# Kernel tuning notes

Hardware: AMD Instinct MI355X
Metric: run time of the kernel (lower is better)

Reference implementation:

```python
import jax, jax.numpy as jnp
import numpy as np

C = 32        # channels
B = 4         # batch
H = W = 256   # spatial
K = 3         # adaptive kernel size
BN_EPS = 1e-5


def conv2d(x, w, b, pad):
    # x: [B,Cin,H,W], w: [Cout,Cin,kh,kw]
    y = jax.lax.conv_general_dilated(
        x, w, window_strides=(1, 1), padding=[(pad, pad), (pad, pad)],
        dimension_numbers=('NCHW', 'OIHW', 'NCHW'))
    return y + b[None, :, None, None]


def bn(x, g, beta, mu, var):
    scale = (g / jnp.sqrt(var + BN_EPS))[None, :, None, None]
    return (x - mu[None, :, None, None]) * scale + beta[None, :, None, None]


def res_block(x, w, b, g, beta, mu, var):
    # w: [2,C,C,3,3]; conv-BN-ReLU-conv-BN, residual add, ReLU
    h = bn(conv2d(x, w[0], b[0], 1), g[0], beta[0], mu[0], var[0])
    h = jax.nn.relu(h)
    h = bn(conv2d(h, w[1], b[1], 1), g[1], beta[1], mu[1], var[1])
    return jax.nn.relu(x + h)


def kernel_pred(frames, core, rate):
    # frames: [B,N,H,W] (color=1 squeezed), core: [B,N,K*K,H,W]
    b, n, h, w = frames.shape
    p = (K // 2) * rate
    fp = jnp.pad(frames, ((0, 0), (0, 0), (p, p), (p, p)))
    # stack K*K shifted copies along new axis 2 (same order as torch loop)
    stack = jnp.stack([fp[:, :, i * rate:i * rate + h, j * rate:j * rate + w]
                       for i in range(K) for j in range(K)], axis=2)
    return jnp.sum(core * stack, axis=2)  # [B,N,H,W]; white_level=1.0


def setup_inputs() -> dict:
    key = jax.random.key(0)
    ks = jax.random.split(key, 16)
    inp = {}
    inp['input'] = jax.random.normal(ks[0], (B, C, H, W), dtype=jnp.float32)
    # 4 residual blocks x 2 convs each
    inp['wconv'] = 0.05 * jax.random.normal(ks[1], (4, 2, C, C, 3, 3), dtype=jnp.float32)
    inp['bconv'] = jnp.zeros((4, 2, C), dtype=jnp.float32)
    inp['bn_gamma'] = jnp.ones((4, 2, C), dtype=jnp.float32) + 0.01 * jax.random.normal(ks[2], (4, 2, C), dtype=jnp.float32)
    inp['bn_beta'] = 0.01 * jax.random.normal(ks[3], (4, 2, C), dtype=jnp.float32)
    inp['bn_mean'] = 0.1 * jax.random.normal(ks[4], (4, 2, C), dtype=jnp.float32)
    inp['bn_var'] = 0.5 + jax.random.uniform(ks[5], (4, 2, C), dtype=jnp.float32)
    inp['tau'] = 0.5 * jnp.ones((1, C, 1, 1), dtype=jnp.float32)
    inp['w_outc'] = 0.05 * jax.random.normal(ks[6], (C * 9, C, 1, 1), dtype=jnp.float32)
    inp['b_outc'] = jnp.zeros((C * 9,), dtype=jnp.float32)
    inp['w_final'] = 0.05 * jax.random.normal(ks[7], (C, C * 4, 3, 3), dtype=jnp.float32)
    inp['b_final'] = jnp.zeros((C,), dtype=jnp.float32)
    return inp


def reference(input, wconv, bconv, bn_gamma, bn_beta, bn_mean, bn_var, tau,
              w_outc, b_outc, w_final, b_final):
    m = input
    for i in range(4):  # fixed small structural loop over residual blocks
        m = res_block(m, wconv[i], bconv[i], bn_gamma[i], bn_beta[i],
                      bn_mean[i], bn_var[i])
    m5 = jax.nn.relu(m - tau)
    core = conv2d(m5, w_outc, b_outc, 0)                    # [B, C*9, H, W]
    core = core.reshape(B, C, K * K, H, W)                  # [B, N, 9, H, W]
    preds = [kernel_pred(input, core, r) for r in (1, 2, 3, 4)]
    pred_cat = jnp.concatenate(preds, axis=1)               # [B, 4C, H, W]
    return conv2d(pred_cat, w_final, b_final, 1)            # [B, C, H, W]
```

## Files before the change

### kernel.cpp

```cpp
#include <hip/hip_runtime.h>

typedef __bf16 bf16;
typedef __attribute__((ext_vector_type(8))) __bf16 bf16x8;
typedef __attribute__((ext_vector_type(4))) float f32x4;

#define HH 256
#define WW 256
#define BB 4
#define NPIX 65536
#define AS 264
#define APX 69696
#define PS 258
#define PPX 66564

#define GLOAD16(SRC, DST) __builtin_amdgcn_global_load_lds( \
    (const __attribute__((address_space(1))) void*)(SRC),   \
    (__attribute__((address_space(3))) void*)(DST), 16, 0, 0)

__device__ inline bf16x8 bzero8() {
    bf16x8 v;
    #pragma unroll
    for (int i = 0; i < 8; ++i) v[i] = (bf16)0.0f;
    return v;
}

__device__ inline int chof(int s) {
    return 4 * (s >> 3) + 16 * ((s >> 2) & 1) + (s & 3);
}

__global__ __launch_bounds__(256) void prep_in(const float* __restrict__ in,
                                               bf16* __restrict__ outP) {
    int p = blockIdx.x * 256 + threadIdx.x;
    int b = p >> 16, rem = p & 65535;
    int y = rem >> 8, x = rem & 255;
    float ch[32];
    #pragma unroll
    for (int c = 0; c < 32; ++c)
        ch[c] = in[(size_t)(b * 32 + c) * NPIX + rem];
    bf16* o = outP + ((size_t)b * APX + (size_t)(y + 4) * AS + x + 4) * 32;
    #pragma unroll
    for (int g = 0; g < 4; ++g) {
        bf16x8 w;
        #pragma unroll
        for (int j = 0; j < 4; ++j) {
            w[j]     = (bf16)ch[4 * g + j];
            w[4 + j] = (bf16)ch[16 + 4 * g + j];
        }
        *reinterpret_cast<bf16x8*>(o + g * 8) = w;
    }
}

__global__ __launch_bounds__(256) void zero_halo(bf16* __restrict__ in0b,
                                                 bf16* __restrict__ actA,
                                                 bf16* __restrict__ actB,
                                                 bf16* __restrict__ pred) {
    int i = blockIdx.x * 256 + threadIdx.x;
    const int NA = 3 * 4 * 4160;
    if (i < NA) {
        int buf = i / (4 * 4160), r = i % (4 * 4160);
        int b = r / 4160, k = r % 4160;
        int y, x;
        if (k < 2112) { int rr = k / 264; y = rr < 4 ? rr : 256 + rr; x = k % 264; }
        else { int j = k - 2112; y = 4 + j / 8; int c8 = j % 8; x = c8 < 4 ? c8 : 256 + c8; }
        bf16* p = (buf == 0 ? in0b : buf == 1 ? actA : actB) +
                  ((size_t)b * APX + (size_t)y * AS + x) * 32;
        #pragma unroll
        for (int cg = 0; cg < 4; ++cg)
            *reinterpret_cast<bf16x8*>(p + cg * 8) = bzero8();
    } else if (i < NA + 4 * 1028) {
        int r = i - NA;
        int b = r / 1028, k = r % 1028;
        int y, x;
        if (k < 516) { int rr = k / 258; y = rr ? 257 : 0; x = k % 258; }
        else { int j = k - 516; y = 1 + j / 2; x = (j & 1) ? 257 : 0; }
        bf16* p = pred + ((size_t)b * PPX + (size_t)y * PS + x) * 128;
        #pragma unroll
        for (int cg = 0; cg < 16; ++cg)
            *reinterpret_cast<bf16x8*>(p + cg * 8) = bzero8();
    }
}

__global__ void fold_w(const float* __restrict__ wconv, const float* __restrict__ bconv,
                       const float* __restrict__ g, const float* __restrict__ beta,
                       const float* __restrict__ mu, const float* __restrict__ var,
                       const float* __restrict__ w_outc, const float* __restrict__ b_outc,
                       const float* __restrict__ w_final, const float* __restrict__ tau,
                       bf16* __restrict__ Wres, float* __restrict__ Bres,
                       bf16* __restrict__ Wcore, bf16* __restrict__ Wfin,
                       float* __restrict__ bCore, float* __restrict__ tauP) {
    int idx = blockIdx.x * 256 + threadIdx.x;
    if (idx < 73728) {
        int l = idx / 9216, r = idx % 9216;
        int tap = r >> 10, co = (r >> 5) & 31, ci = chof(r & 31);
        float s = g[l * 32 + co] * rsqrtf(var[l * 32 + co] + 1e-5f);
        Wres[idx] = (bf16)(wconv[l * 9216 + (co * 32 + ci) * 9 + tap] * s);
    } else if (idx < 73984) {
        int i = idx - 73728;
        float s = g[i] * rsqrtf(var[i] + 1e-5f);
        Bres[i] = (bconv[i] - mu[i]) * s + beta[i];
    } else if (idx < 83200) {
        int r = idx - 73984;
        int tap = r >> 10, nn = (r >> 5) & 31, ci = chof(r & 31);
        Wcore[r] = (bf16)w_outc[(nn * 9 + tap) * 32 + ci];
    } else if (idx < 120064) {
        int r = idx - 83200;
        int chunk = r / 9216, r2 = r % 9216;
        int tap = r2 >> 10, co = (r2 >> 5) & 31, n = chof(r2 & 31);
        Wfin[r] = (bf16)w_final[(size_t)(co * 128 + chunk * 32 + n) * 9 + tap];
    } else if (idx < 120352) {
        int r = idx - 120064;
        int tap = r >> 5, n = r & 31;
        bCore[r] = b_outc[n * 9 + tap];
    } else if (idx < 120384) {
        int s = idx - 120352;
        tauP[s] = tau[chof(s)];
    }
}

__global__ __launch_bounds__(512) void resblock_v4(
    const bf16* __restrict__ in, const bf16* __restrict__ W1,
    const bf16* __restrict__ W2, const float* __restrict__ B1,
    const float* __restrict__ B2, bf16* __restrict__ out) {
    extern __shared__ char smem[];
    bf16* xs = (bf16*)smem;
    bf16* hs = (bf16*)(smem + 52224);
    const int x0 = blockIdx.x * 64, y0 = blockIdx.y * 8, b = blockIdx.z;
    const int tid = threadIdx.x;
    const int lane = tid & 63, wv = tid >> 6;
    const int col = lane & 15, g = lane >> 4;
    const bf16* inb = in + (size_t)b * APX * 32;

    for (int gi = wv; gi < 51; gi += 8) {
        int i = gi * 64 + lane;
        int px = i >> 2, s = i & 3;
        int yy = px / 68, xx = px % 68;
        int gsl = s ^ ((px >> 1) & 3);
        const bf16* src = inb + ((size_t)(y0 + yy + 2) * AS + x0 + xx + 2) * 32 + gsl * 8;
        GLOAD16(src, smem + gi * 1024);
    }

    bf16x8 Wf[9][2];
    #pragma unroll
    for (int tap = 0; tap < 9; ++tap) {
        Wf[tap][0] = *reinterpret_cast<const bf16x8*>(W1 + tap * 1024 + col * 32 + g * 8);
        Wf[tap][1] = *reinterpret_cast<const bf16x8*>(W1 + tap * 1024 + (16 + col) * 32 + g * 8);
    }
    f32x4 bb0 = *reinterpret_cast<const f32x4*>(B1 + 4 * g);
    f32x4 bb1 = *reinterpret_cast<const f32x4*>(B1 + 16 + 4 * g);
    __syncthreads();

    for (int id = wv; id < 15; id += 8) {
        int u = id / 5, s5 = id % 5;
        int rb = u * 4; if (rb > 6) rb = 6;
        int off = s5 * 16; if (off > 50) off = 50;
        f32x4 c[4][2];
        #pragma unroll
        for (int rr = 0; rr < 4; ++rr) { c[rr][0] = bb0; c[rr][1] = bb1; }
        #pragma unroll
        for (int d = 0; d < 6; ++d) {
            #pragma unroll
            for (int dx = 0; dx < 3; ++dx) {
                const int px = (rb + d) * 68 + off + col + dx;
                bf16x8 Bf = *reinterpret_cast<const bf16x8*>(
                    xs + px * 32 + (g ^ ((px >> 1) & 3)) * 8);
                #pragma unroll
                for (int rr = 0; rr < 4; ++rr) {
                    if (rr <= d && d - rr <= 2) {
                        const int tap = (d - rr) * 3 + dx;
                        c[rr][0] = __builtin_amdgcn_mfma_f32_16x16x32_bf16(Wf[tap][0], Bf, c[rr][0], 0, 0, 0);
                        c[rr][1] = __builtin_amdgcn_mfma_f32_16x16x32_bf16(Wf[tap][1], Bf, c[rr][1], 0, 0, 0);
                    }
                }
            }
        }
        #pragma unroll
        for (int rr = 0; rr < 4; ++rr) {
            bf16x8 o;
            #pragma unroll
            for (int j = 0; j < 4; ++j) {
                o[j]     = (bf16)fmaxf(c[rr][0][j], 0.0f);
                o[4 + j] = (bf16)fmaxf(c[rr][1][j], 0.0f);
            }
            const int hy = y0 + rb + rr - 1;
            const int hx = x0 + off + col - 1;
            if ((unsigned)hy >= HH || (unsigned)hx >= WW) o = bzero8();
            *reinterpret_cast<bf16x8*>(hs + ((rb + rr) * 66 + off + col) * 40 + g * 8) = o;
        }
    }

    #pragma unroll
    for (int tap = 0; tap < 9; ++tap) {
        Wf[tap][0] = *reinterpret_cast<const bf16x8*>(W2 + tap * 1024 + col * 32 + g * 8);
        Wf[tap][1] = *reinterpret_cast<const bf16x8*>(W2 + tap * 1024 + (16 + col) * 32 + g * 8);
    }
    bb0 = *reinterpret_cast<const f32x4*>(B2 + 4 * g);
    bb1 = *reinterpret_cast<const f32x4*>(B2 + 16 + 4 * g);
    __syncthreads();

    {
        const int rb2 = (wv >> 2) * 4, seg = (wv & 3) * 16;
        f32x4 c[4][2];
        #pragma unroll
        for (int rr = 0; rr < 4; ++rr) { c[rr][0] = bb0; c[rr][1] = bb1; }
        #pragma unroll
        for (int d = 0; d < 6; ++d) {
            #pragma unroll
            for (int dx = 0; dx < 3; ++dx) {
                bf16x8 Bf = *reinterpret_cast<const bf16x8*>(
                    hs + ((rb2 + d) * 66 + seg + col + dx) * 40 + g * 8);
                #pragma unroll
                for (int rr = 0; rr < 4; ++rr) {
                    if (rr <= d && d - rr <= 2) {
                        const int tap = (d - rr) * 3 + dx;
                        c[rr][0] = __builtin_amdgcn_mfma_f32_16x16x32_bf16(Wf[tap][0], Bf, c[rr][0], 0, 0, 0);
                        c[rr][1] = __builtin_amdgcn_mfma_f32_16x16x32_bf16(Wf[tap][1], Bf, c[rr][1], 0, 0, 0);
                    }
                }
            }
        }
        bf16* outb = out + (size_t)b * APX * 32;
        #pragma unroll
        for (int rr = 0; rr < 4; ++rr) {
            const int y = rb2 + rr;
            const int pxr = (y + 2) * 68 + seg + col + 2;
            bf16x8 xr = *reinterpret_cast<const bf16x8*>(
                xs + pxr * 32 + (g ^ ((pxr >> 1) & 3)) * 8);
            bf16x8 o;
            #pragma unroll
            for (int j = 0; j < 4; ++j) {
                o[j]     = (bf16)fmaxf(c[rr][0][j] + (float)xr[j], 0.0f);
                o[4 + j] = (bf16)fmaxf(c[rr][1][j] + (float)xr[4 + j], 0.0f);
            }
            *reinterpret_cast<bf16x8*>(
                outb + ((size_t)(y0 + y + 4) * AS + x0 + seg + col + 4) * 32 + g * 8) = o;
        }
    }
}

__global__ __launch_bounds__(512) void final_conv_v6(
    const bf16* __restrict__ pred, const bf16* __restrict__ Wfin,
    const float* __restrict__ bfin, float* __restrict__ out) {
    extern __shared__ char smem[];
    const int x0 = blockIdx.x * 64, y0 = blockIdx.y * 8, b = blockIdx.z;
    const int tid = threadIdx.x;
    const int lane = tid & 63, wv = tid >> 6;
    const int col = lane & 15, g = lane >> 4;
    const bf16* pb = pred + (size_t)b * PPX * 128;

    auto stage = [&](int c, int bi) {
        for (int gi = wv; gi < 42; gi += 8) {
            int i = gi * 64 + lane;
            int px = i >> 2; if (px > 659) px = 659;
            int s = i & 3;
            int yy = px / 66, xx = px % 66;
            int gsl = s ^ ((px >> 1) & 3);
            const bf16* src = pb + ((size_t)(y0 + yy) * PS + x0 + xx) * 128 + c * 32 + gsl * 8;
            GLOAD16(src, smem + bi * 43008 + gi * 1024);
        }
    };

    const int rb = (wv >> 2) * 4, seg = (wv & 3) * 16;
    f32x4 a[4][2];
    {
        f32x4 b0 = *reinterpret_cast<const f32x4*>(bfin + 4 * g);
        f32x4 b1 = *reinterpret_cast<const f32x4*>(bfin + 16 + 4 * g);
        #pragma unroll
        for (int rr = 0; rr < 4; ++rr) { a[rr][0] = b0; a[rr][1] = b1; }
    }

    stage(0, 0);
    __syncthreads();

    for (int chunk = 0; chunk < 4; ++chunk) {
        const int cur = chunk & 1;
        bf16x8 Wf[9][2];
        #pragma unroll
        for (int tap = 0; tap < 9; ++tap) {
            Wf[tap][0] = *reinterpret_cast<const bf16x8*>(
                Wfin + chunk * 9216 + tap * 1024 + col * 32 + g * 8);
            Wf[tap][1] = *reinterpret_cast<const bf16x8*>(
                Wfin + chunk * 9216 + tap * 1024 + (16 + col) * 32 + g * 8);
        }
        if (chunk < 3) stage(chunk + 1, cur ^ 1);

        const bf16* pt = (const bf16*)(smem + cur * 43008);
        #pragma unroll
        for (int d = 0; d < 6; ++d) {
            #pragma unroll
            for (int dx = 0; dx < 3; ++dx) {
                const int px = (rb + d) * 66 + seg + col + dx;
                bf16x8 Bf = *reinterpret_cast<const bf16x8*>(
                    pt + px * 32 + (g ^ ((px >> 1) & 3)) * 8);
                #pragma unroll
                for (int rr = 0; rr < 4; ++rr) {
                    if (rr <= d && d - rr <= 2) {
                        const int tap = (d - rr) * 3 + dx;
                        a[rr][0] = __builtin_amdgcn_mfma_f32_16x16x32_bf16(Wf[tap][0], Bf, a[rr][0], 0, 0, 0);
                        a[rr][1] = __builtin_amdgcn_mfma_f32_16x16x32_bf16(Wf[tap][1], Bf, a[rr][1], 0, 0, 0);
                    }
                }
            }
        }
        __syncthreads();
    }

    #pragma unroll
    for (int rr = 0; rr < 4; ++rr) {
        const int y = y0 + rb + rr;
        const int x = x0 + seg + col;
        #pragma unroll
        for (int j = 0; j < 4; ++j) {
            out[(size_t)(b * 32 + 4 * g + j) * NPIX + (size_t)y * WW + x] = a[rr][0][j];
            out[(size_t)(b * 32 + 16 + 4 * g + j) * NPIX + (size_t)y * WW + x] = a[rr][1][j];
        }
    }
}

__global__ __launch_bounds__(256, 2) void core_pred_v4(
    const bf16* __restrict__ m, const bf16* __restrict__ framesP,
    const float* __restrict__ tauP, const bf16* __restrict__ WcoreG,
    const float* __restrict__ bCore, bf16* __restrict__ pred) {
    __shared__ bf16 fr[576 * 32];
    __shared__ bf16 Wc[9 * 32 * 32];
    const int x0 = blockIdx.x * 16, y0 = blockIdx.y * 16, b = blockIdx.z;
    const int tid = threadIdx.x;
    const int lane = tid & 63, wv = tid >> 6;
    const int col = lane & 15, g = lane >> 4;

    for (int i = tid; i < 1152; i += 256)
        *reinterpret_cast<bf16x8*>(Wc + i * 8) =
            *reinterpret_cast<const bf16x8*>(WcoreG + i * 8);
    const bf16* fb = framesP + (size_t)b * APX * 32;
    for (int i = tid; i < 2304; i += 256) {
        int px = i >> 2, cg = i & 3;
        int yy = px / 24, xx = px % 24;
        bf16x8 v = *reinterpret_cast<const bf16x8*>(
            fb + ((size_t)(y0 + yy) * AS + x0 + xx) * 32 + cg * 8);
        *reinterpret_cast<bf16x8*>(fr + px * 32 + cg * 8) = v;
    }
    float t8[8];
    #pragma unroll
    for (int k = 0; k < 8; ++k) t8[k] = tauP[g * 8 + k];
    __syncthreads();

    const bf16* mb = m + (size_t)b * APX * 32;
    bf16* pb = pred + (size_t)b * PPX * 128;

    #pragma unroll 1
    for (int uu = 0; uu < 4; ++uu) {
        const int yl = wv * 4 + uu;
        const int y = y0 + yl;

        bf16x8 Bv = *reinterpret_cast<const bf16x8*>(
            mb + ((size_t)(y + 4) * AS + x0 + col + 4) * 32 + g * 8);
        #pragma unroll
        for (int k = 0; k < 8; ++k)
            Bv[k] = (bf16)fmaxf((float)Bv[k] - t8[k], 0.0f);

        float acc[4][8];
        #pragma unroll
        for (int r = 0; r < 4; ++r)
            #pragma unroll
            for (int k = 0; k < 8; ++k) acc[r][k] = 0.0f;

        #pragma unroll
        for (int dy = 0; dy < 3; ++dy) {
            float core[3][8];
            #pragma unroll
            for (int dx = 0; dx < 3; ++dx) {
                const int tap = dy * 3 + dx;
                bf16x8 A0 = *reinterpret_cast<const bf16x8*>(
                    Wc + tap * 1024 + col * 32 + g * 8);
                bf16x8 A1 = *reinterpret_cast<const bf16x8*>(
                    Wc + tap * 1024 + (16 + col) * 32 + g * 8);
                f32x4 c0 = *reinterpret_cast<const f32x4*>(bCore + tap * 32 + 4 * g);
                f32x4 c1 = *reinterpret_cast<const f32x4*>(bCore + tap * 32 + 16 + 4 * g);
                c0 = __builtin_amdgcn_mfma_f32_16x16x32_bf16(A0, Bv, c0, 0, 0, 0);
                c1 = __builtin_amdgcn_mfma_f32_16x16x32_bf16(A1, Bv, c1, 0, 0, 0);
                #pragma unroll
                for (int j = 0; j < 4; ++j) {
                    core[dx][j]     = c0[j];
                    core[dx][4 + j] = c1[j];
                }
            }
            #pragma unroll
            for (int r = 1; r <= 4; ++r) {
                const int row = yl + 4 + (dy - 1) * r;
                #pragma unroll
                for (int dx = 0; dx < 3; ++dx) {
                    const int cc = col + 4 + (dx - 1) * r;
                    bf16x8 f8 = *reinterpret_cast<const bf16x8*>(
                        fr + (row * 24 + cc) * 32 + g * 8);
                    #pragma unroll
                    for (int k = 0; k < 8; ++k)
                        acc[r - 1][k] += core[dx][k] * (float)f8[k];
                }
            }
        }

        #pragma unroll
        for (int r = 0; r < 4; ++r) {
            bf16x8 o;
            #pragma unroll
            for (int k = 0; k < 8; ++k) o[k] = (bf16)acc[r][k];
            *reinterpret_cast<bf16x8*>(
                pb + ((size_t)(y + 1) * PS + x0 + col + 1) * 128 + r * 32 + g * 8) = o;
        }
    }
}

extern "C" void kernel_launch(void* const* d_in, const int* in_sizes, int n_in,
                              void* d_out, int out_size, void* d_ws, size_t ws_size,
                              hipStream_t stream) {
    const float* input    = (const float*)d_in[0];
    const float* wconv    = (const float*)d_in[1];
    const float* bconv    = (const float*)d_in[2];
    const float* bn_gamma = (const float*)d_in[3];
    const float* bn_beta  = (const float*)d_in[4];
    const float* bn_mean  = (const float*)d_in[5];
    const float* bn_var   = (const float*)d_in[6];
    const float* tau      = (const float*)d_in[7];
    const float* w_outc   = (const float*)d_in[8];
    const float* b_outc   = (const float*)d_in[9];
    const float* w_final  = (const float*)d_in[10];
    const float* b_final  = (const float*)d_in[11];
    float* out = (float*)d_out;

    char* ws = (char*)d_ws;
    bf16*  Wres  = (bf16*)(ws);
    float* Bres  = (float*)(ws + 147456);
    bf16*  Wcore = (bf16*)(ws + 148480);
    bf16*  Wfin  = (bf16*)(ws + 166912);
    float* bCore = (float*)(ws + 240640);
    float* tauP  = (float*)(ws + 241792);
    const size_t ACTB = (size_t)APX * 32 * 2;
    bf16*  in0b  = (bf16*)(ws + 245760);
    bf16*  actA  = (bf16*)(ws + 245760 + 4 * ACTB);
    bf16*  actB  = (bf16*)(ws + 245760 + 8 * ACTB);
    bf16*  pred  = (bf16*)(ws + 245760 + 12 * ACTB);

    hipFuncSetAttribute(reinterpret_cast<const void*>(&resblock_v4),
                        hipFuncAttributeMaxDynamicSharedMemorySize, 105024);
    hipFuncSetAttribute(reinterpret_cast<const void*>(&final_conv_v6),
                        hipFuncAttributeMaxDynamicSharedMemorySize, 86016);

    prep_in<<<1024, 256, 0, stream>>>(input, in0b);
    zero_halo<<<212, 256, 0, stream>>>(in0b, actA, actB, pred);
    fold_w<<<471, 256, 0, stream>>>(wconv, bconv, bn_gamma, bn_beta, bn_mean, bn_var,
                                    w_outc, b_outc, w_final, tau,
                                    Wres, Bres, Wcore, Wfin, bCore, tauP);

    dim3 gridr(4, 32, 4), blkr(512);
    resblock_v4<<<gridr, blkr, 105024, stream>>>(in0b, Wres + 0 * 9216, Wres + 1 * 9216,
                                                 Bres + 0,  Bres + 32,  actA);
    resblock_v4<<<gridr, blkr, 105024, stream>>>(actA, Wres + 2 * 9216, Wres + 3 * 9216,
                                                 Bres + 64, Bres + 96,  actB);
    resblock_v4<<<gridr, blkr, 105024, stream>>>(actB, Wres + 4 * 9216, Wres + 5 * 9216,
                                                 Bres + 128, Bres + 160, actA);
    resblock_v4<<<gridr, blkr, 105024, stream>>>(actA, Wres + 6 * 9216, Wres + 7 * 9216,
                                                 Bres + 192, Bres + 224, actB);

    dim3 gridp(16, 16, 4);
    core_pred_v4<<<gridp, dim3(256), 0, stream>>>(actB, in0b, tauP, Wcore, bCore, pred);

    dim3 gridf(4, 32, 4);
    final_conv_v6<<<gridf, dim3(512), 86016, stream>>>(pred, Wfin, b_final, out);
}
```

Measured before the change: 177.1 us.

## Fuse core prediction and final conv into one kernel via LDS pred tile

Merges the adaptive-kernel prediction stage and the final 3x3 conv into a single kernel. Each 16x16 tile computes the 128-channel pred values, including a one-pixel halo, directly into shared memory, then runs the final conv from there. This removes the global write and re-read of the bf16 pred tensor and one kernel launch. The cost is halo recomputation (18x18 against 16x16 pixels, about 27% extra core work) and a large LDS footprint (~126 KB), which limits occupancy.

```diff
diff --git a/kernel.cpp b/kernel.cpp
--- a/kernel.cpp
+++ b/kernel.cpp
@@ -52,8 +52,7 @@
 
 __global__ __launch_bounds__(256) void zero_halo(bf16* __restrict__ in0b,
                                                  bf16* __restrict__ actA,
-                                                 bf16* __restrict__ actB,
-                                                 bf16* __restrict__ pred) {
+                                                 bf16* __restrict__ actB) {
     int i = blockIdx.x * 256 + threadIdx.x;
     const int NA = 3 * 4 * 4160;
     if (i < NA) {
@@ -66,16 +65,6 @@
                   ((size_t)b * APX + (size_t)y * AS + x) * 32;
         #pragma unroll
         for (int cg = 0; cg < 4; ++cg)
-            *reinterpret_cast<bf16x8*>(p + cg * 8) = bzero8();
-    } else if (i < NA + 4 * 1028) {
-        int r = i - NA;
-        int b = r / 1028, k = r % 1028;
-        int y, x;
-        if (k < 516) { int rr = k / 258; y = rr ? 257 : 0; x = k % 258; }
-        else { int j = k - 516; y = 1 + j / 2; x = (j & 1) ? 257 : 0; }
-        bf16* p = pred + ((size_t)b * PPX + (size_t)y * PS + x) * 128;
-        #pragma unroll
-        for (int cg = 0; cg < 16; ++cg)
             *reinterpret_cast<bf16x8*>(p + cg * 8) = bzero8();
     }
 }
@@ -237,42 +226,115 @@
     }
 }
 
-__global__ __launch_bounds__(512) void final_conv_v6(
-    const bf16* __restrict__ pred, const bf16* __restrict__ Wfin,
+__global__ __launch_bounds__(512) void core_final(
+    const bf16* __restrict__ m, const bf16* __restrict__ framesP,
+    const float* __restrict__ tauP, const bf16* __restrict__ WcoreG,
+    const float* __restrict__ bCore, const bf16* __restrict__ Wfin,
     const float* __restrict__ bfin, float* __restrict__ out) {
     extern __shared__ char smem[];
-    const int x0 = blockIdx.x * 64, y0 = blockIdx.y * 8, b = blockIdx.z;
+    bf16* fr    = (bf16*)smem;
+    bf16* predt = (bf16*)(smem + 43264);
+    const int x0 = blockIdx.x * 16, y0 = blockIdx.y * 16, b = blockIdx.z;
     const int tid = threadIdx.x;
     const int lane = tid & 63, wv = tid >> 6;
     const int col = lane & 15, g = lane >> 4;
-    const bf16* pb = pred + (size_t)b * PPX * 128;
-
-    auto stage = [&](int c, int bi) {
-        for (int gi = wv; gi < 42; gi += 8) {
-            int i = gi * 64 + lane;
-            int px = i >> 2; if (px > 659) px = 659;
-            int s = i & 3;
-            int yy = px / 66, xx = px % 66;
-            int gsl = s ^ ((px >> 1) & 3);
-            const bf16* src = pb + ((size_t)(y0 + yy) * PS + x0 + xx) * 128 + c * 32 + gsl * 8;
-            GLOAD16(src, smem + bi * 43008 + gi * 1024);
-        }
-    };
-
-    const int rb = (wv >> 2) * 4, seg = (wv & 3) * 16;
-    f32x4 a[4][2];
+
+    const bf16* fb = framesP + (size_t)b * APX * 32;
+    for (int i = tid; i < 2704; i += 512) {
+        int rec = i >> 2, c = i & 3;
+        int yy = rec / 26, xx = rec % 26;
+        int gy = y0 + yy - 5, gx = x0 + xx - 5;
+        bf16x8 v = bzero8();
+        if ((unsigned)gy < HH && (unsigned)gx < WW)
+            v = *reinterpret_cast<const bf16x8*>(
+                fb + ((size_t)(gy + 4) * AS + gx + 4) * 32 + c * 8);
+        *reinterpret_cast<bf16x8*>(fr + rec * 32 + (c ^ ((rec >> 1) & 3)) * 8) = v;
+    }
+
+    bf16x8 Ac[9][2];
+    #pragma unroll
+    for (int tap = 0; tap < 9; ++tap) {
+        Ac[tap][0] = *reinterpret_cast<const bf16x8*>(WcoreG + tap * 1024 + col * 32 + g * 8);
+        Ac[tap][1] = *reinterpret_cast<const bf16x8*>(WcoreG + tap * 1024 + (16 + col) * 32 + g * 8);
+    }
+    float t8[8];
+    #pragma unroll
+    for (int k = 0; k < 8; ++k) t8[k] = tauP[g * 8 + k];
+    __syncthreads();
+
+    const bf16* mb = m + (size_t)b * APX * 32;
+    for (int u = wv; u < 36; u += 8) {
+        const int pr = u >> 1, cg = u & 1;
+        const int pc = cg * 2 + col;
+        const int gy = y0 - 1 + pr, gx = x0 - 1 + pc;
+
+        bf16x8 Bv = *reinterpret_cast<const bf16x8*>(
+            mb + ((size_t)(gy + 4) * AS + gx + 4) * 32 + g * 8);
+        #pragma unroll
+        for (int k = 0; k < 8; ++k)
+            Bv[k] = (bf16)fmaxf((float)Bv[k] - t8[k], 0.0f);
+
+        float acc[4][8];
+        #pragma unroll
+        for (int r = 0; r < 4; ++r)
+            #pragma unroll
+            for (int k = 0; k < 8; ++k) acc[r][k] = 0.0f;
+
+        #pragma unroll
+        for (int dy = 0; dy < 3; ++dy) {
+            float core[3][8];
+            #pragma unroll
+            for (int dx = 0; dx < 3; ++dx) {
+                const int tap = dy * 3 + dx;
+                f32x4 c0 = *reinterpret_cast<const f32x4*>(bCore + tap * 32 + 4 * g);
+                f32x4 c1 = *reinterpret_cast<const f32x4*>(bCore + tap * 32 + 16 + 4 * g);
+                c0 = __builtin_amdgcn_mfma_f32_16x16x32_bf16(Ac[tap][0], Bv, c0, 0, 0, 0);
+                c1 = __builtin_amdgcn_mfma_f32_16x16x32_bf16(Ac[tap][1], Bv, c1, 0, 0, 0);
+                #pragma unroll
+                for (int j = 0; j < 4; ++j) {
+                    core[dx][j]     = c0[j];
+                    core[dx][4 + j] = c1[j];
+                }
+            }
+            #pragma unroll
+            for (int R = 1; R <= 4; ++R) {
+                const int fy = pr + 4 + (dy - 1) * R;
+                #pragma unroll
+                for (int dx = 0; dx < 3; ++dx) {
+                    const int fx = pc + 4 + (dx - 1) * R;
+                    const int rec = fy * 26 + fx;
+                    bf16x8 f8 = *reinterpret_cast<const bf16x8*>(
+                        fr + rec * 32 + (g ^ ((rec >> 1) & 3)) * 8);
+                    #pragma unroll
+                    for (int k = 0; k < 8; ++k)
+                        acc[R - 1][k] += core[dx][k] * (float)f8[k];
+                }
+            }
+        }
+
+        const bool oob = ((unsigned)gy >= HH) || ((unsigned)gx >= WW);
+        const int px = pr * 18 + pc;
+        #pragma unroll
+        for (int r = 0; r < 4; ++r) {
+            bf16x8 o;
+            #pragma unroll
+            for (int k = 0; k < 8; ++k) o[k] = oob ? (bf16)0.0f : (bf16)acc[r][k];
+            *reinterpret_cast<bf16x8*>(
+                predt + px * 128 + ((r * 4 + g) ^ (px & 7)) * 8) = o;
+        }
+    }
+    __syncthreads();
+
+    const int rb = wv * 2;
+    f32x4 a[2][2];
     {
         f32x4 b0 = *reinterpret_cast<const f32x4*>(bfin + 4 * g);
         f32x4 b1 = *reinterpret_cast<const f32x4*>(bfin + 16 + 4 * g);
         #pragma unroll
-        for (int rr = 0; rr < 4; ++rr) { a[rr][0] = b0; a[rr][1] = b1; }
-    }
-
-    stage(0, 0);
-    __syncthreads();
+        for (int rr = 0; rr < 2; ++rr) { a[rr][0] = b0; a[rr][1] = b1; }
+    }
 
     for (int chunk = 0; chunk < 4; ++chunk) {
-        const int cur = chunk & 1;
         bf16x8 Wf[9][2];
         #pragma unroll
         for (int tap = 0; tap < 9; ++tap) {
@@ -281,18 +343,15 @@
             Wf[tap][1] = *reinterpret_cast<const bf16x8*>(
                 Wfin + chunk * 9216 + tap * 1024 + (16 + col) * 32 + g * 8);
         }
-        if (chunk < 3) stage(chunk + 1, cur ^ 1);
-
-        const bf16* pt = (const bf16*)(smem + cur * 43008);
-        #pragma unroll
-        for (int d = 0; d < 6; ++d) {
+        #pragma unroll
+        for (int d = 0; d < 4; ++d) {
             #pragma unroll
             for (int dx = 0; dx < 3; ++dx) {
-                const int px = (rb + d) * 66 + seg + col + dx;
+                const int px = (rb + d) * 18 + col + dx;
                 bf16x8 Bf = *reinterpret_cast<const bf16x8*>(
-                    pt + px * 32 + (g ^ ((px >> 1) & 3)) * 8);
+                    predt + px * 128 + (((chunk * 4 + g) ^ (px & 7))) * 8);
                 #pragma unroll
-                for (int rr = 0; rr < 4; ++rr) {
+                for (int rr = 0; rr < 2; ++rr) {
                     if (rr <= d && d - rr <= 2) {
                         const int tap = (d - rr) * 3 + dx;
                         a[rr][0] = __builtin_amdgcn_mfma_f32_16x16x32_bf16(Wf[tap][0], Bf, a[rr][0], 0, 0, 0);
@@ -301,110 +360,16 @@
                 }
             }
         }
-        __syncthreads();
-    }
-
-    #pragma unroll
-    for (int rr = 0; rr < 4; ++rr) {
+    }
+
+    #pragma unroll
+    for (int rr = 0; rr < 2; ++rr) {
         const int y = y0 + rb + rr;
-        const int x = x0 + seg + col;
+        const int x = x0 + col;
         #pragma unroll
         for (int j = 0; j < 4; ++j) {
             out[(size_t)(b * 32 + 4 * g + j) * NPIX + (size_t)y * WW + x] = a[rr][0][j];
             out[(size_t)(b * 32 + 16 + 4 * g + j) * NPIX + (size_t)y * WW + x] = a[rr][1][j];
-        }
-    }
-}
-
-__global__ __launch_bounds__(256, 2) void core_pred_v4(
-    const bf16* __restrict__ m, const bf16* __restrict__ framesP,
-    const float* __restrict__ tauP, const bf16* __restrict__ WcoreG,
-    const float* __restrict__ bCore, bf16* __restrict__ pred) {
-    __shared__ bf16 fr[576 * 32];
-    __shared__ bf16 Wc[9 * 32 * 32];
-    const int x0 = blockIdx.x * 16, y0 = blockIdx.y * 16, b = blockIdx.z;
-    const int tid = threadIdx.x;
-    const int lane = tid & 63, wv = tid >> 6;
-    const int col = lane & 15, g = lane >> 4;
-
-    for (int i = tid; i < 1152; i += 256)
-        *reinterpret_cast<bf16x8*>(Wc + i * 8) =
-            *reinterpret_cast<const bf16x8*>(WcoreG + i * 8);
-    const bf16* fb = framesP + (size_t)b * APX * 32;
-    for (int i = tid; i < 2304; i += 256) {
-        int px = i >> 2, cg = i & 3;
-        int yy = px / 24, xx = px % 24;
-        bf16x8 v = *reinterpret_cast<const bf16x8*>(
-            fb + ((size_t)(y0 + yy) * AS + x0 + xx) * 32 + cg * 8);
-        *reinterpret_cast<bf16x8*>(fr + px * 32 + cg * 8) = v;
-    }
-    float t8[8];
-    #pragma unroll
-    for (int k = 0; k < 8; ++k) t8[k] = tauP[g * 8 + k];
-    __syncthreads();
-
-    const bf16* mb = m + (size_t)b * APX * 32;
-    bf16* pb = pred + (size_t)b * PPX * 128;
-
-    #pragma unroll 1
-    for (int uu = 0; uu < 4; ++uu) {
-        const int yl = wv * 4 + uu;
-        const int y = y0 + yl;
-
-        bf16x8 Bv = *reinterpret_cast<const bf16x8*>(
-            mb + ((size_t)(y + 4) * AS + x0 + col + 4) * 32 + g * 8);
-        #pragma unroll
-        for (int k = 0; k < 8; ++k)
-            Bv[k] = (bf16)fmaxf((float)Bv[k] - t8[k], 0.0f);
-
-        float acc[4][8];
-        #pragma unroll
-        for (int r = 0; r < 4; ++r)
-            #pragma unroll
-            for (int k = 0; k < 8; ++k) acc[r][k] = 0.0f;
-
-        #pragma unroll
-        for (int dy = 0; dy < 3; ++dy) {
-            float core[3][8];
-            #pragma unroll
-            for (int dx = 0; dx < 3; ++dx) {
-                const int tap = dy * 3 + dx;
-                bf16x8 A0 = *reinterpret_cast<const bf16x8*>(
-                    Wc + tap * 1024 + col * 32 + g * 8);
-                bf16x8 A1 = *reinterpret_cast<const bf16x8*>(
-                    Wc + tap * 1024 + (16 + col) * 32 + g * 8);
-                f32x4 c0 = *reinterpret_cast<const f32x4*>(bCore + tap * 32 + 4 * g);
-                f32x4 c1 = *reinterpret_cast<const f32x4*>(bCore + tap * 32 + 16 + 4 * g);
-                c0 = __builtin_amdgcn_mfma_f32_16x16x32_bf16(A0, Bv, c0, 0, 0, 0);
-                c1 = __builtin_amdgcn_mfma_f32_16x16x32_bf16(A1, Bv, c1, 0, 0, 0);
-                #pragma unroll
-                for (int j = 0; j < 4; ++j) {
-                    core[dx][j]     = c0[j];
-                    core[dx][4 + j] = c1[j];
-                }
-            }
-            #pragma unroll
-            for (int r = 1; r <= 4; ++r) {
-                const int row = yl + 4 + (dy - 1) * r;
-                #pragma unroll
-                for (int dx = 0; dx < 3; ++dx) {
-                    const int cc = col + 4 + (dx - 1) * r;
-                    bf16x8 f8 = *reinterpret_cast<const bf16x8*>(
-                        fr + (row * 24 + cc) * 32 + g * 8);
-                    #pragma unroll
-                    for (int k = 0; k < 8; ++k)
-                        acc[r - 1][k] += core[dx][k] * (float)f8[k];
-                }
-            }
-        }
-
-        #pragma unroll
-        for (int r = 0; r < 4; ++r) {
-            bf16x8 o;
-            #pragma unroll
-            for (int k = 0; k < 8; ++k) o[k] = (bf16)acc[r][k];
-            *reinterpret_cast<bf16x8*>(
-                pb + ((size_t)(y + 1) * PS + x0 + col + 1) * 128 + r * 32 + g * 8) = o;
         }
     }
 }
@@ -437,15 +402,14 @@
     bf16*  in0b  = (bf16*)(ws + 245760);
     bf16*  actA  = (bf16*)(ws + 245760 + 4 * ACTB);
     bf16*  actB  = (bf16*)(ws + 245760 + 8 * ACTB);
-    bf16*  pred  = (bf16*)(ws + 245760 + 12 * ACTB);
 
     hipFuncSetAttribute(reinterpret_cast<const void*>(&resblock_v4),
                         hipFuncAttributeMaxDynamicSharedMemorySize, 105024);
-    hipFuncSetAttribute(reinterpret_cast<const void*>(&final_conv_v6),
-                        hipFuncAttributeMaxDynamicSharedMemorySize, 86016);
+    hipFuncSetAttribute(reinterpret_cast<const void*>(&core_final),
+                        hipFuncAttributeMaxDynamicSharedMemorySize, 126208);
 
     prep_in<<<1024, 256, 0, stream>>>(input, in0b);
-    zero_halo<<<212, 256, 0, stream>>>(in0b, actA, actB, pred);
+    zero_halo<<<195, 256, 0, stream>>>(in0b, actA, actB);
     fold_w<<<471, 256, 0, stream>>>(wconv, bconv, bn_gamma, bn_beta, bn_mean, bn_var,
                                     w_outc, b_outc, w_final, tau,
                                     Wres, Bres, Wcore, Wfin, bCore, tauP);
@@ -460,9 +424,7 @@
     resblock_v4<<<gridr, blkr, 105024, stream>>>(actA, Wres + 6 * 9216, Wres + 7 * 9216,
                                                  Bres + 192, Bres + 224, actB);
 
-    dim3 gridp(16, 16, 4);
-    core_pred_v4<<<gridp, dim3(256), 0, stream>>>(actB, in0b, tauP, Wcore, bCore, pred);
-
-    dim3 gridf(4, 32, 4);
-    final_conv_v6<<<gridf, dim3(512), 86016, stream>>>(pred, Wfin, b_final, out);
-}
+    dim3 gridcf(16, 16, 4);
+    core_final<<<gridcf, dim3(512), 126208, stream>>>(actB, in0b, tauP, Wcore, bCore,
+                                                      Wfin, b_final, out);
+}
```

New measurement: 505.8 us. +185.5%, slower.
